# Optimization experiments

Hardware: AMD Instinct MI355X
Metric: run time of the kernel (lower is better)

## Reference

```python
import jax, jax.numpy as jnp
import numpy as np
from jax import lax

N, C, H, W = 16384, 1, 28, 28
HID = 128
EPS = 1e-5


def setup_inputs() -> dict:
    key = jax.random.key(0)
    ks = jax.random.split(key, 12)
    x = jax.random.normal(ks[0], (N, C, H, W), jnp.float32)
    w1 = jax.random.normal(ks[1], (8, 1, 7, 7), jnp.float32) * 0.05
    g1 = 1.0 + 0.1 * jax.random.normal(ks[2], (8,), jnp.float32)
    b1 = 0.1 * jax.random.normal(ks[3], (8,), jnp.float32)
    w2 = jax.random.normal(ks[4], (10, 8, 5, 5), jnp.float32) * 0.05
    g2 = 1.0 + 0.1 * jax.random.normal(ks[5], (10,), jnp.float32)
    b2 = 0.1 * jax.random.normal(ks[6], (10,), jnp.float32)
    w3 = jax.random.normal(ks[7], (HID, 10, 1, 1), jnp.float32) * 0.05
    g3 = 1.0 + 0.1 * jax.random.normal(ks[8], (HID,), jnp.float32)
    b3 = 0.1 * jax.random.normal(ks[9], (HID,), jnp.float32)
    # original inits fc weight to 0 and bias to identity affine; we add a small
    # random weight so theta varies per sample (exercises the sampler)
    fw = jax.random.normal(ks[10], (6, HID), jnp.float32) * 0.01
    fb = jnp.array([1, 0, 0, 0, 1, 0], jnp.float32)
    return {"x": x, "w1": w1, "g1": g1, "b1": b1, "w2": w2, "g2": g2,
            "b2": b2, "w3": w3, "g3": g3, "b3": b3, "fw": fw, "fb": fb}


def conv2d(x, w):
    return lax.conv_general_dilated(x, w, (1, 1), 'VALID',
                                    dimension_numbers=('NCHW', 'OIHW', 'NCHW'))


def batchnorm(x, g, b):
    m = jnp.mean(x, axis=(0, 2, 3), keepdims=True)
    v = jnp.mean((x - m) ** 2, axis=(0, 2, 3), keepdims=True)
    xh = (x - m) * lax.rsqrt(v + EPS)
    return xh * g[None, :, None, None] + b[None, :, None, None]


def maxpool2(x):
    return lax.reduce_window(x, -jnp.inf, lax.max, (1, 1, 2, 2), (1, 1, 2, 2), 'VALID')


def bilinear_sample(img_nhwc, grid):
    # img_nhwc: [N,H,W,C], grid: [N,H,W,2] normalized coords (x, y) in [-1,1]
    ix = (grid[..., 0] + 1.0) * 0.5 * (W - 1)
    iy = (grid[..., 1] + 1.0) * 0.5 * (H - 1)
    x0f = jnp.floor(ix); y0f = jnp.floor(iy)
    wx = ix - x0f; wy = iy - y0f
    x0 = jnp.clip(x0f.astype(jnp.int32), 0, W - 1)
    x1 = jnp.clip(x0 + 1, 0, W - 1)
    y0 = jnp.clip(y0f.astype(jnp.int32), 0, H - 1)
    y1 = jnp.clip(y0 + 1, 0, H - 1)

    def gather(img, yy, xx):  # img [H,W,C], yy/xx [H,W] -> [H,W,C]
        return img[yy, xx]
    g = jax.vmap(gather)
    v00 = g(img_nhwc, y0, x0)
    v01 = g(img_nhwc, y0, x1)
    v10 = g(img_nhwc, y1, x0)
    v11 = g(img_nhwc, y1, x1)
    wx = wx[..., None]; wy = wy[..., None]
    top = v00 * (1 - wx) + v01 * wx
    bot = v10 * (1 - wx) + v11 * wx
    return top * (1 - wy) + bot * wy


def reference(x, w1, g1, b1, w2, g2, b2, w3, g3, b3, fw, fb):
    # localization network
    xs = jax.nn.relu(maxpool2(batchnorm(conv2d(x, w1), g1, b1)))   # [N,8,11,11]
    xs = jax.nn.relu(maxpool2(batchnorm(conv2d(xs, w2), g2, b2)))  # [N,10,3,3]
    xs = jax.nn.relu(batchnorm(conv2d(xs, w3), g3, b3))            # [N,128,3,3]
    xs = jnp.mean(xs, axis=(2, 3))                                 # avgpool 3x3 -> [N,128]
    theta = (xs @ fw.T + fb).reshape(-1, 2, 3)                     # [N,2,3]
    # affine grid over normalized coords
    lin_x = jnp.linspace(-1.0, 1.0, W)
    lin_y = jnp.linspace(-1.0, 1.0, H)
    gx, gy = jnp.meshgrid(lin_x, lin_y)                            # [H,W]
    base = jnp.stack([gx, gy, jnp.ones_like(gx)], axis=-1)         # [H,W,3]
    grid = jnp.einsum('nij,hwj->nhwi', theta, base)                # [N,H,W,2]
    # sample in NHWC (matches the transpose dance in the torch code)
    out = bilinear_sample(jnp.transpose(x, (0, 2, 3, 1)), grid)
    return jnp.transpose(out, (0, 3, 1, 2))                        # back to NCHW
```

## Files before the change

kernel.cpp:

```cpp
#include <hip/hip_runtime.h>


static constexpr float kEPS = 1e-5f;

#define O_SUM1 0
#define O_SSQ1 8
#define O_SUM2 16
#define O_SSQ2 26
#define O_MOM  36
#define O_W2T  104
#define O_THETA 2112
#define O_E1   100864
#define O_E2   15960576

__global__ __launch_bounds__(256) void k_init(const float* __restrict__ w2,
                                              float* __restrict__ ws){
  int i = blockIdx.x*256 + threadIdx.x;
  if (i < 104) ws[i] = 0.f;
  if (i < 2000){
    int ic = i & 7;
    int r  = i >> 3;
    int kx = r % 5; r /= 5;
    int ky = r % 5; r /= 5;
    int oc = r;
    ws[O_W2T + i] = w2[(oc*8 + ic)*25 + ky*5 + kx];
  }
}

__global__ __launch_bounds__(256) void k_conv1(const float* __restrict__ x,
                                               const float* __restrict__ w1,
                                               const float* __restrict__ g1,
                                               float* __restrict__ ws){
  __shared__ float sw[392];
  const int tid = threadIdx.x;
  for (int i = tid; i < 392; i += 256) sw[i] = w1[i];
  __syncthreads();
  const int gid = blockIdx.x*256 + tid;
  const int ph = gid & 1;
  const int c  = (gid >> 1) & 7;
  const int n  = gid >> 4;
  const float* __restrict__ xs = x + n*784;
  const float* __restrict__ wc = sw + c*49;
  const bool pos = (g1[c] >= 0.f);
  float sum=0.f, ssq=0.f;
  float* __restrict__ outp = ws + O_E1 + n*968 + c;
  const int p0 = ph*6;
  const int p1 = ph ? 11 : 6;
  for (int p=p0; p<p1; p++){
    float a0[22], a1[22];
    #pragma unroll
    for (int i=0;i<22;i++){ a0[i]=0.f; a1[i]=0.f; }
    #pragma unroll
    for (int j=0;j<8;j++){
      float in[28];
      const float4* __restrict__ rp = (const float4*)(xs + (2*p+j)*28);
      #pragma unroll
      for (int q=0;q<7;q++){
        float4 v = rp[q];
        in[4*q]=v.x; in[4*q+1]=v.y; in[4*q+2]=v.z; in[4*q+3]=v.w;
      }
      if (j < 7){
        #pragma unroll
        for (int kx=0;kx<7;kx++){
          float wv = wc[j*7+kx];
          #pragma unroll
          for (int xo=0;xo<22;xo++) a0[xo] = fmaf(wv, in[xo+kx], a0[xo]);
        }
      }
      if (j >= 1){
        #pragma unroll
        for (int kx=0;kx<7;kx++){
          float wv = wc[(j-1)*7+kx];
          #pragma unroll
          for (int xo=0;xo<22;xo++) a1[xo] = fmaf(wv, in[xo+kx], a1[xo]);
        }
      }
    }
    #pragma unroll
    for (int xo=0;xo<22;xo++){
      sum += a0[xo] + a1[xo];
      ssq = fmaf(a0[xo],a0[xo],ssq);
      ssq = fmaf(a1[xo],a1[xo],ssq);
    }
    #pragma unroll
    for (int px=0;px<11;px++){
      float m4 = fmaxf(fmaxf(a0[2*px],a0[2*px+1]), fmaxf(a1[2*px],a1[2*px+1]));
      float n4 = fminf(fminf(a0[2*px],a0[2*px+1]), fminf(a1[2*px],a1[2*px+1]));
      outp[(p*11+px)*8] = pos ? m4 : n4;
    }
  }
  sum += __shfl_xor(sum,1);  ssq += __shfl_xor(ssq,1);
  sum += __shfl_xor(sum,16); ssq += __shfl_xor(ssq,16);
  sum += __shfl_xor(sum,32); ssq += __shfl_xor(ssq,32);
  __shared__ float ls[16];
  if (tid < 16) ls[tid] = 0.f;
  __syncthreads();
  int l = tid & 63;
  if ((l & 0x31) == 0){
    atomicAdd(&ls[l>>1], sum);
    atomicAdd(&ls[8 + (l>>1)], ssq);
  }
  __syncthreads();
  if (tid < 16) atomicAdd(&ws[O_SUM1 + tid], ls[tid]);
}

__global__ __launch_bounds__(256) void k_conv2(float* __restrict__ ws,
                                               const float* __restrict__ g1,
                                               const float* __restrict__ b1,
                                               const float* __restrict__ g2){
  float s1r[8], t1r[8];
  {
    const float invM1 = 1.f/7929856.f;
    #pragma unroll
    for (int c=0;c<8;c++){
      float mean = ws[O_SUM1+c]*invM1;
      float var  = ws[O_SSQ1+c]*invM1 - mean*mean;
      float sc = g1[c]*rsqrtf(var + kEPS);
      s1r[c] = sc; t1r[c] = b1[c] - mean*sc;
    }
  }
  const int blk = blockIdx.x;
  const int half = (blk >= 640) ? 1 : 0;
  const int gid = (blk - half*640)*256 + threadIdx.x;
  const int n = gid/10, oc = gid - 10*n;
  const int r0 = half*4;
  const int nrows = half ? 7 : 8;
  const float* __restrict__ wt = ws + O_W2T + oc*200;
  const float* __restrict__ base = ws + O_E1 + n*968;
  float acc[28];
  #pragma unroll
  for (int i=0;i<28;i++) acc[i]=0.f;
  for (int jj=0; jj<nrows; ++jj){
    const int iy = r0 + jj;
    float in[88];
    const float4* __restrict__ rp = (const float4*)(base + iy*88);
    #pragma unroll
    for (int q=0;q<22;q++){
      float4 v = rp[q];
      in[4*q+0] = fmaxf(fmaf(s1r[(4*q+0)&7], v.x, t1r[(4*q+0)&7]), 0.f);
      in[4*q+1] = fmaxf(fmaf(s1r[(4*q+1)&7], v.y, t1r[(4*q+1)&7]), 0.f);
      in[4*q+2] = fmaxf(fmaf(s1r[(4*q+2)&7], v.z, t1r[(4*q+2)&7]), 0.f);
      in[4*q+3] = fmaxf(fmaf(s1r[(4*q+3)&7], v.w, t1r[(4*q+3)&7]), 0.f);
    }
    #pragma unroll
    for (int ol=0; ol<4; ++ol){
      if (half && ol==3) continue;
      const int ky = jj - ol;
      if (ky < 0 || ky > 4) continue;
      const float* __restrict__ wrow = wt + ky*40;
      #pragma unroll
      for (int kx=0;kx<5;kx++){
        float4 wa = *(const float4*)(wrow + kx*8);
        float4 wb = *(const float4*)(wrow + kx*8 + 4);
        #pragma unroll
        for (int ox=0;ox<7;ox++){
          float a = acc[ol*7+ox];
          a = fmaf(wa.x, in[(ox+kx)*8+0], a);
          a = fmaf(wa.y, in[(ox+kx)*8+1], a);
          a = fmaf(wa.z, in[(ox+kx)*8+2], a);
          a = fmaf(wa.w, in[(ox+kx)*8+3], a);
          a = fmaf(wb.x, in[(ox+kx)*8+4], a);
          a = fmaf(wb.y, in[(ox+kx)*8+5], a);
          a = fmaf(wb.z, in[(ox+kx)*8+6], a);
          a = fmaf(wb.w, in[(ox+kx)*8+7], a);
          acc[ol*7+ox] = a;
        }
      }
    }
  }
  {
    const int NV = (half ? 3 : 4)*7;
    float sum=0.f, ssq=0.f;
    #pragma unroll
    for (int i=0;i<28;i++){
      if (i < NV){ float v = acc[i]; sum += v; ssq = fmaf(v,v,ssq); }
    }
    __shared__ float ls[20];
    if (threadIdx.x < 20) ls[threadIdx.x] = 0.f;
    __syncthreads();
    atomicAdd(&ls[oc], sum);
    atomicAdd(&ls[10+oc], ssq);
    __syncthreads();
    if (threadIdx.x < 20) atomicAdd(&ws[O_SUM2 + threadIdx.x], ls[threadIdx.x]);
  }
  {
    const bool pos = (g2[oc] >= 0.f);
    const int npy = half ? 1 : 2;
    #pragma unroll
    for (int pl=0; pl<2; pl++){
      if (pl >= npy) continue;
      const int py = half ? 2 : pl;
      #pragma unroll
      for (int px=0;px<3;px++){
        float v00 = acc[(2*pl)*7   + 2*px], v01 = acc[(2*pl)*7   + 2*px+1];
        float v10 = acc[(2*pl+1)*7 + 2*px], v11 = acc[(2*pl+1)*7 + 2*px+1];
        float m4 = fmaxf(fmaxf(v00,v01), fmaxf(v10,v11));
        float n4 = fminf(fminf(v00,v01), fminf(v10,v11));
        ws[O_E2 + (n*9 + py*3 + px)*10 + oc] = pos ? m4 : n4;
      }
    }
  }
}

__global__ __launch_bounds__(256) void k_pool2fin(float* __restrict__ ws,
                                                  const float* __restrict__ g2,
                                                  const float* __restrict__ b2){
  __shared__ float smom[65];
  const int tid = threadIdx.x;
  if (tid < 65) smom[tid] = 0.f;
  __syncthreads();
  const float invM = 1.f/802816.f;
  const int gid = blockIdx.x*256 + tid;
  float* __restrict__ p = ws + O_E2 + gid*10;
  float xv[10];
  #pragma unroll
  for (int c=0;c<10;c++){
    float mean = ws[O_SUM2+c]*invM;
    float var  = ws[O_SSQ2+c]*invM - mean*mean;
    float sc = g2[c]*rsqrtf(var + kEPS);
    float tc = b2[c] - mean*sc;
    float v = fmaxf(fmaf(sc, p[c], tc), 0.f);
    xv[c] = v;
    p[c] = v;
  }
  float mu[10], sm[55];
  #pragma unroll
  for (int i=0;i<10;i++) mu[i] = xv[i];
  #pragma unroll
  for (int i=0;i<10;i++){
    #pragma unroll
    for (int j=i;j<10;j++) sm[i*10 - i*(i-1)/2 + (j-i)] = xv[i]*xv[j];
  }
  #pragma unroll
  for (int off=1; off<64; off<<=1){
    #pragma unroll
    for (int i=0;i<10;i++) mu[i] += __shfl_xor(mu[i], off);
    #pragma unroll
    for (int k=0;k<55;k++) sm[k] += __shfl_xor(sm[k], off);
  }
  if ((tid & 63) == 0){
    #pragma unroll
    for (int i=0;i<10;i++) atomicAdd(&smom[i], mu[i]);
    #pragma unroll
    for (int k=0;k<55;k++) atomicAdd(&smom[10+k], sm[k]);
  }
  __syncthreads();
  if (tid < 65) atomicAdd(&ws[O_MOM + tid], smom[tid]);
}

__global__ __launch_bounds__(256) void k_theta(float* __restrict__ ws,
                                               const float* __restrict__ w3,
                                               const float* __restrict__ g3,
                                               const float* __restrict__ b3,
                                               const float* __restrict__ fw,
                                               const float* __restrict__ fb){
  __shared__ float s3[128], t3[128];
  const int tid = threadIdx.x;
  if (tid < 128){
    const int oc = tid;
    const float invM = 1.f/147456.f;
    float mu[10], w[10];
    #pragma unroll
    for (int i=0;i<10;i++) mu[i] = ws[O_MOM+i]*invM;
    #pragma unroll
    for (int i=0;i<10;i++) w[i] = w3[oc*10+i];
    float mean3 = 0.f;
    #pragma unroll
    for (int i=0;i<10;i++) mean3 += w[i]*mu[i];
    float var3 = 0.f;
    #pragma unroll
    for (int i=0;i<10;i++){
      #pragma unroll
      for (int j=i;j<10;j++){
        float Sij = ws[O_MOM+10 + i*10 - i*(i-1)/2 + (j-i)]*invM;
        float cov = Sij - mu[i]*mu[j];
        float coef = (i==j) ? 1.f : 2.f;
        var3 += coef * w[i] * w[j] * cov;
      }
    }
    var3 = fmaxf(var3, 0.f);
    float s = g3[oc]*rsqrtf(var3 + kEPS);
    s3[oc] = s;
    t3[oc] = b3[oc] - mean3*s;
  }
  __syncthreads();
  const int n = blockIdx.x*256 + tid;
  const float* __restrict__ ip = ws + O_E2 + n*90;
  float in[90];
  #pragma unroll
  for (int i=0;i<90;i++) in[i] = ip[i];
  float th[6];
  #pragma unroll
  for (int j=0;j<6;j++) th[j] = fb[j];
  for (int oc=0; oc<128; oc++){
    float s = s3[oc], t = t3[oc];
    float fsum = 0.f;
    #pragma unroll
    for (int p=0;p<9;p++){
      float v = 0.f;
      #pragma unroll
      for (int ic=0;ic<10;ic++) v = fmaf(w3[oc*10+ic], in[p*10+ic], v);
      fsum += fmaxf(fmaf(s,v,t), 0.f);
    }
    float feat = fsum * (1.f/9.f);
    #pragma unroll
    for (int j=0;j<6;j++) th[j] = fmaf(fw[j*128+oc], feat, th[j]);
  }
  float* __restrict__ op = ws + O_THETA + n*6;
  #pragma unroll
  for (int j=0;j<6;j++) op[j] = th[j];
}

__global__ __launch_bounds__(256) void k_sample(const float* __restrict__ x,
                                                const float* __restrict__ ws,
                                                float* __restrict__ out){
  const int n = blockIdx.x;
  __shared__ float sx[784];
  const int tid = threadIdx.x;
  if (tid < 196) ((float4*)sx)[tid] = ((const float4*)(x + n*784))[tid];
  __syncthreads();
  const float* __restrict__ th = ws + O_THETA + n*6;
  const float t0=th[0], t1=th[1], t2=th[2], t3=th[3], t4=th[4], t5=th[5];
  float* __restrict__ op = out + n*784;
  for (int idx=tid; idx<784; idx+=256){
    int h = idx/28;
    int wcol = idx - 28*h;
    float gx = fmaf((float)wcol, 2.f/27.f, -1.f);
    float gy = fmaf((float)h,    2.f/27.f, -1.f);
    float ix = (fmaf(t0,gx,fmaf(t1,gy,t2)) + 1.f)*13.5f;
    float iy = (fmaf(t3,gx,fmaf(t4,gy,t5)) + 1.f)*13.5f;
    float x0f = floorf(ix), y0f = floorf(iy);
    float wx = ix - x0f, wy = iy - y0f;
    int x0 = min(max((int)x0f,0),27); int x1 = min(x0+1,27);
    int y0 = min(max((int)y0f,0),27); int y1 = min(y0+1,27);
    float v00 = sx[y0*28+x0], v01 = sx[y0*28+x1];
    float v10 = sx[y1*28+x0], v11 = sx[y1*28+x1];
    float top = v00*(1.f-wx) + v01*wx;
    float bot = v10*(1.f-wx) + v11*wx;
    op[idx] = top*(1.f-wy) + bot*wy;
  }
}

extern "C" void kernel_launch(void* const* d_in, const int* in_sizes, int n_in,
                              void* d_out, int out_size, void* d_ws, size_t ws_size,
                              hipStream_t stream){
  (void)in_sizes; (void)n_in; (void)out_size; (void)ws_size;
  const float* x  = (const float*)d_in[0];
  const float* w1 = (const float*)d_in[1];
  const float* g1 = (const float*)d_in[2];
  const float* b1 = (const float*)d_in[3];
  const float* w2 = (const float*)d_in[4];
  const float* g2 = (const float*)d_in[5];
  const float* b2 = (const float*)d_in[6];
  const float* w3 = (const float*)d_in[7];
  const float* g3 = (const float*)d_in[8];
  const float* b3 = (const float*)d_in[9];
  const float* fw = (const float*)d_in[10];
  const float* fb = (const float*)d_in[11];
  float* ws  = (float*)d_ws;
  float* out = (float*)d_out;

  hipLaunchKernelGGL(k_init,      dim3(8),     dim3(256), 0, stream, w2, ws);
  hipLaunchKernelGGL(k_conv1,     dim3(1024),  dim3(256), 0, stream, x, w1, g1, ws);
  hipLaunchKernelGGL(k_conv2,     dim3(1280),  dim3(256), 0, stream, ws, g1, b1, g2);
  hipLaunchKernelGGL(k_pool2fin,  dim3(576),   dim3(256), 0, stream, ws, g2, b2);
  hipLaunchKernelGGL(k_theta,     dim3(64),    dim3(256), 0, stream, ws, w3, g3, b3, fw, fb);
  hipLaunchKernelGGL(k_sample,    dim3(16384), dim3(256), 0, stream, x, ws, out);
}
```

Baseline: 399.1 us.

## Cut register pressure in conv kernels, stage conv2 weights in LDS, transpose theta input

conv1 now computes each output row in two 11-wide halves instead of one 22-wide pass, which lowers register use. conv2 copies its weights into padded shared memory and processes input channels in two groups of four, which shrinks its input register array. pool2fin writes its normalized activations in a channel-major transposed layout, so k_theta can do coalesced per-sample loads. k_theta is also relaunched with 64-thread blocks over 256 blocks to spread work across more CUs. The costs are extra shared-memory traffic, a second workspace region, and strided stores in pool2fin.

```diff
diff --git a/kernel.cpp b/kernel.cpp
--- a/kernel.cpp
+++ b/kernel.cpp
@@ -12,6 +12,7 @@
 #define O_THETA 2112
 #define O_E1   100864
 #define O_E2   15960576
+#define O_E2T  17435136
 
 __global__ __launch_bounds__(256) void k_init(const float* __restrict__ w2,
                                               float* __restrict__ ws){
@@ -47,46 +48,77 @@
   const int p0 = ph*6;
   const int p1 = ph ? 11 : 6;
   for (int p=p0; p<p1; p++){
-    float a0[22], a1[22];
-    #pragma unroll
-    for (int i=0;i<22;i++){ a0[i]=0.f; a1[i]=0.f; }
-    #pragma unroll
-    for (int j=0;j<8;j++){
-      float in[28];
-      const float4* __restrict__ rp = (const float4*)(xs + (2*p+j)*28);
-      #pragma unroll
-      for (int q=0;q<7;q++){
-        float4 v = rp[q];
-        in[4*q]=v.x; in[4*q+1]=v.y; in[4*q+2]=v.z; in[4*q+3]=v.w;
-      }
-      if (j < 7){
+    float cm = 0.f, cn = 0.f;
+    #pragma unroll
+    for (int h=0; h<2; h++){
+      float a0[11], a1[11];
+      #pragma unroll
+      for (int i=0;i<11;i++){ a0[i]=0.f; a1[i]=0.f; }
+      #pragma unroll
+      for (int j=0;j<8;j++){
+        float in[17];
+        const float* __restrict__ rb = xs + (2*p+j)*28 + 11*h;
+        if (h==0){
+          const float4* __restrict__ rp = (const float4*)rb;
+          float4 v0=rp[0], v1=rp[1], v2=rp[2], v3=rp[3];
+          in[0]=v0.x; in[1]=v0.y; in[2]=v0.z; in[3]=v0.w;
+          in[4]=v1.x; in[5]=v1.y; in[6]=v1.z; in[7]=v1.w;
+          in[8]=v2.x; in[9]=v2.y; in[10]=v2.z; in[11]=v2.w;
+          in[12]=v3.x; in[13]=v3.y; in[14]=v3.z; in[15]=v3.w;
+          in[16]=rb[16];
+        } else {
+          in[0]=rb[0];
+          const float4* __restrict__ rp = (const float4*)(rb+1);
+          float4 v0=rp[0], v1=rp[1], v2=rp[2], v3=rp[3];
+          in[1]=v0.x; in[2]=v0.y; in[3]=v0.z; in[4]=v0.w;
+          in[5]=v1.x; in[6]=v1.y; in[7]=v1.z; in[8]=v1.w;
+          in[9]=v2.x; in[10]=v2.y; in[11]=v2.z; in[12]=v2.w;
+          in[13]=v3.x; in[14]=v3.y; in[15]=v3.z; in[16]=v3.w;
+        }
+        if (j < 7){
+          #pragma unroll
+          for (int kx=0;kx<7;kx++){
+            float wv = wc[j*7+kx];
+            #pragma unroll
+            for (int xo=0;xo<11;xo++) a0[xo] = fmaf(wv, in[xo+kx], a0[xo]);
+          }
+        }
+        if (j >= 1){
+          #pragma unroll
+          for (int kx=0;kx<7;kx++){
+            float wv = wc[(j-1)*7+kx];
+            #pragma unroll
+            for (int xo=0;xo<11;xo++) a1[xo] = fmaf(wv, in[xo+kx], a1[xo]);
+          }
+        }
+      }
+      #pragma unroll
+      for (int xo=0;xo<11;xo++){
+        sum += a0[xo] + a1[xo];
+        ssq = fmaf(a0[xo],a0[xo],ssq);
+        ssq = fmaf(a1[xo],a1[xo],ssq);
+      }
+      if (h==0){
         #pragma unroll
-        for (int kx=0;kx<7;kx++){
-          float wv = wc[j*7+kx];
-          #pragma unroll
-          for (int xo=0;xo<22;xo++) a0[xo] = fmaf(wv, in[xo+kx], a0[xo]);
-        }
-      }
-      if (j >= 1){
+        for (int px=0;px<5;px++){
+          float m4 = fmaxf(fmaxf(a0[2*px],a0[2*px+1]), fmaxf(a1[2*px],a1[2*px+1]));
+          float n4 = fminf(fminf(a0[2*px],a0[2*px+1]), fminf(a1[2*px],a1[2*px+1]));
+          outp[(p*11+px)*8] = pos ? m4 : n4;
+        }
+        cm = fmaxf(a0[10], a1[10]);
+        cn = fminf(a0[10], a1[10]);
+      } else {
+        float m4 = fmaxf(cm, fmaxf(a0[0],a1[0]));
+        float n4 = fminf(cn, fminf(a0[0],a1[0]));
+        outp[(p*11+5)*8] = pos ? m4 : n4;
         #pragma unroll
-        for (int kx=0;kx<7;kx++){
-          float wv = wc[(j-1)*7+kx];
-          #pragma unroll
-          for (int xo=0;xo<22;xo++) a1[xo] = fmaf(wv, in[xo+kx], a1[xo]);
-        }
-      }
-    }
-    #pragma unroll
-    for (int xo=0;xo<22;xo++){
-      sum += a0[xo] + a1[xo];
-      ssq = fmaf(a0[xo],a0[xo],ssq);
-      ssq = fmaf(a1[xo],a1[xo],ssq);
-    }
-    #pragma unroll
-    for (int px=0;px<11;px++){
-      float m4 = fmaxf(fmaxf(a0[2*px],a0[2*px+1]), fmaxf(a1[2*px],a1[2*px+1]));
-      float n4 = fminf(fminf(a0[2*px],a0[2*px+1]), fminf(a1[2*px],a1[2*px+1]));
-      outp[(p*11+px)*8] = pos ? m4 : n4;
+        for (int q=0;q<5;q++){
+          int l0 = 1+2*q, l1 = 2+2*q;
+          float m4q = fmaxf(fmaxf(a0[l0],a0[l1]), fmaxf(a1[l0],a1[l1]));
+          float n4q = fminf(fminf(a0[l0],a0[l1]), fminf(a1[l0],a1[l1]));
+          outp[(p*11+6+q)*8] = pos ? m4q : n4q;
+        }
+      }
     }
   }
   sum += __shfl_xor(sum,1);  ssq += __shfl_xor(ssq,1);
@@ -108,6 +140,12 @@
                                                const float* __restrict__ g1,
                                                const float* __restrict__ b1,
                                                const float* __restrict__ g2){
+  __shared__ float sw2[2160];
+  for (int i = threadIdx.x; i < 2000; i += 256){
+    int oc_ = i/200, r = i - oc_*200;
+    sw2[oc_*216 + r] = ws[O_W2T + i];
+  }
+  __syncthreads();
   float s1r[8], t1r[8];
   {
     const float invM1 = 1.f/7929856.f;
@@ -125,45 +163,42 @@
   const int n = gid/10, oc = gid - 10*n;
   const int r0 = half*4;
   const int nrows = half ? 7 : 8;
-  const float* __restrict__ wt = ws + O_W2T + oc*200;
+  const float* __restrict__ wt = sw2 + oc*216;
   const float* __restrict__ base = ws + O_E1 + n*968;
   float acc[28];
   #pragma unroll
   for (int i=0;i<28;i++) acc[i]=0.f;
   for (int jj=0; jj<nrows; ++jj){
     const int iy = r0 + jj;
-    float in[88];
-    const float4* __restrict__ rp = (const float4*)(base + iy*88);
-    #pragma unroll
-    for (int q=0;q<22;q++){
-      float4 v = rp[q];
-      in[4*q+0] = fmaxf(fmaf(s1r[(4*q+0)&7], v.x, t1r[(4*q+0)&7]), 0.f);
-      in[4*q+1] = fmaxf(fmaf(s1r[(4*q+1)&7], v.y, t1r[(4*q+1)&7]), 0.f);
-      in[4*q+2] = fmaxf(fmaf(s1r[(4*q+2)&7], v.z, t1r[(4*q+2)&7]), 0.f);
-      in[4*q+3] = fmaxf(fmaf(s1r[(4*q+3)&7], v.w, t1r[(4*q+3)&7]), 0.f);
-    }
-    #pragma unroll
-    for (int ol=0; ol<4; ++ol){
-      if (half && ol==3) continue;
-      const int ky = jj - ol;
-      if (ky < 0 || ky > 4) continue;
-      const float* __restrict__ wrow = wt + ky*40;
-      #pragma unroll
-      for (int kx=0;kx<5;kx++){
-        float4 wa = *(const float4*)(wrow + kx*8);
-        float4 wb = *(const float4*)(wrow + kx*8 + 4);
+    #pragma unroll
+    for (int icl=0; icl<2; ++icl){
+      float4 in4[11];
+      #pragma unroll
+      for (int q=0;q<11;q++){
+        float4 v = *(const float4*)(base + iy*88 + q*8 + icl*4);
+        in4[q].x = fmaxf(fmaf(s1r[icl*4+0], v.x, t1r[icl*4+0]), 0.f);
+        in4[q].y = fmaxf(fmaf(s1r[icl*4+1], v.y, t1r[icl*4+1]), 0.f);
+        in4[q].z = fmaxf(fmaf(s1r[icl*4+2], v.z, t1r[icl*4+2]), 0.f);
+        in4[q].w = fmaxf(fmaf(s1r[icl*4+3], v.w, t1r[icl*4+3]), 0.f);
+      }
+      #pragma unroll
+      for (int ol=0; ol<4; ++ol){
+        if (half && ol==3) continue;
+        const int ky = jj - ol;
+        if (ky < 0 || ky > 4) continue;
+        const float* __restrict__ wrow = wt + ky*40 + icl*4;
         #pragma unroll
-        for (int ox=0;ox<7;ox++){
-          float a = acc[ol*7+ox];
-          a = fmaf(wa.x, in[(ox+kx)*8+0], a);
-          a = fmaf(wa.y, in[(ox+kx)*8+1], a);
-          a = fmaf(wa.z, in[(ox+kx)*8+2], a);
-          a = fmaf(wa.w, in[(ox+kx)*8+3], a);
-          a = fmaf(wb.x, in[(ox+kx)*8+4], a);
-          a = fmaf(wb.y, in[(ox+kx)*8+5], a);
-          a = fmaf(wb.z, in[(ox+kx)*8+6], a);
-          a = fmaf(wb.w, in[(ox+kx)*8+7], a);
-          acc[ol*7+ox] = a;
+        for (int kx=0;kx<5;kx++){
+          float4 w = *(const float4*)(wrow + kx*8);
+          #pragma unroll
+          for (int ox=0;ox<7;ox++){
+            float a = acc[ol*7+ox];
+            a = fmaf(w.x, in4[ox+kx].x, a);
+            a = fmaf(w.y, in4[ox+kx].y, a);
+            a = fmaf(w.z, in4[ox+kx].z, a);
+            a = fmaf(w.w, in4[ox+kx].w, a);
+            acc[ol*7+ox] = a;
+          }
         }
       }
     }
@@ -211,7 +246,8 @@
   __syncthreads();
   const float invM = 1.f/802816.f;
   const int gid = blockIdx.x*256 + tid;
-  float* __restrict__ p = ws + O_E2 + gid*10;
+  const int n = gid/9, p = gid - n*9;
+  const float* __restrict__ src = ws + O_E2 + gid*10;
   float xv[10];
   #pragma unroll
   for (int c=0;c<10;c++){
@@ -219,9 +255,9 @@
     float var  = ws[O_SSQ2+c]*invM - mean*mean;
     float sc = g2[c]*rsqrtf(var + kEPS);
     float tc = b2[c] - mean*sc;
-    float v = fmaxf(fmaf(sc, p[c], tc), 0.f);
+    float v = fmaxf(fmaf(sc, src[c], tc), 0.f);
     xv[c] = v;
-    p[c] = v;
+    ws[O_E2T + (p*10 + c)*16384 + n] = v;
   }
   float mu[10], sm[55];
   #pragma unroll
@@ -248,16 +284,17 @@
   if (tid < 65) atomicAdd(&ws[O_MOM + tid], smom[tid]);
 }
 
-__global__ __launch_bounds__(256) void k_theta(float* __restrict__ ws,
-                                               const float* __restrict__ w3,
-                                               const float* __restrict__ g3,
-                                               const float* __restrict__ b3,
-                                               const float* __restrict__ fw,
-                                               const float* __restrict__ fb){
+__global__ __launch_bounds__(64) void k_theta(float* __restrict__ ws,
+                                              const float* __restrict__ w3,
+                                              const float* __restrict__ g3,
+                                              const float* __restrict__ b3,
+                                              const float* __restrict__ fw,
+                                              const float* __restrict__ fb){
   __shared__ float s3[128], t3[128];
   const int tid = threadIdx.x;
-  if (tid < 128){
-    const int oc = tid;
+  #pragma unroll
+  for (int rep=0; rep<2; rep++){
+    const int oc = tid + rep*64;
     const float invM = 1.f/147456.f;
     float mu[10], w[10];
     #pragma unroll
@@ -284,11 +321,10 @@
     t3[oc] = b3[oc] - mean3*s;
   }
   __syncthreads();
-  const int n = blockIdx.x*256 + tid;
-  const float* __restrict__ ip = ws + O_E2 + n*90;
+  const int n = blockIdx.x*64 + tid;
   float in[90];
   #pragma unroll
-  for (int i=0;i<90;i++) in[i] = ip[i];
+  for (int i=0;i<90;i++) in[i] = ws[O_E2T + i*16384 + n];
   float th[6];
   #pragma unroll
   for (int j=0;j<6;j++) th[j] = fb[j];
@@ -364,6 +400,6 @@
   hipLaunchKernelGGL(k_conv1,     dim3(1024),  dim3(256), 0, stream, x, w1, g1, ws);
   hipLaunchKernelGGL(k_conv2,     dim3(1280),  dim3(256), 0, stream, ws, g1, b1, g2);
   hipLaunchKernelGGL(k_pool2fin,  dim3(576),   dim3(256), 0, stream, ws, g2, b2);
-  hipLaunchKernelGGL(k_theta,     dim3(64),    dim3(256), 0, stream, ws, w3, g3, b3, fw, fb);
+  hipLaunchKernelGGL(k_theta,     dim3(256),   dim3(64),  0, stream, ws, w3, g3, b3, fw, fb);
   hipLaunchKernelGGL(k_sample,    dim3(16384), dim3(256), 0, stream, x, ws, out);
 }
```

New measurement: 434.7 us. 1.09x slower.
